# Kernel optimization log

Hardware: AMD Instinct MI355X
Metric: run time of the kernel (lower is better)

## Reference

```python
import jax, jax.numpy as jnp
import numpy as np

N = 65536   # number of input points
M = 4096    # subsample_size (centroids)
K = 64      # group_limit (neighborhood size)
RADIUS = 0.2  # group_radius


def _mlp(x, W1, b1, W2, b2, W3, b3):
    # PyG MLP([6, 64, 64, 128], act='relu'); batch_norm with default running
    # stats (mean 0, var 1) is identity, so: Linear-ReLU-Linear-ReLU-Linear.
    h = jax.nn.relu(x @ W1 + b1)
    h = jax.nn.relu(h @ W2 + b2)
    return h @ W3 + b3


def setup_inputs() -> dict:
    key = jax.random.key(0)
    ks = jax.random.split(key, 8)
    vertices = jax.random.normal(ks[0], (N, 3), dtype=jnp.float32)
    centroid_indices = jax.random.randint(ks[1], (M,), 0, N)

    def lin(k, fi, fo):
        return (jax.random.normal(k, (fi, fo), dtype=jnp.float32) / np.sqrt(fi)).astype(jnp.float32)

    return {
        "vertices": vertices,
        "centroid_indices": centroid_indices,
        "W1": lin(ks[2], 6, 64),  "b1": jnp.zeros((64,), jnp.float32),
        "W2": lin(ks[3], 64, 64), "b2": jnp.zeros((64,), jnp.float32),
        "W3": lin(ks[4], 64, 128), "b3": jnp.zeros((128,), jnp.float32),
    }


def reference(vertices, centroid_indices, W1, b1, W2, b2, W3, b3):
    # --- group_around_centroids ---
    sq_norm = jnp.einsum('ij,ij->i', vertices, vertices)          # [N]
    cpos = vertices[centroid_indices]                              # [M,3]
    # faithful distance formula: sqrt(|sn_c - 2 c.v + sn|)
    d = jnp.sqrt(jnp.abs(sq_norm[centroid_indices][:, None]
                         - 2.0 * (cpos @ vertices.T)
                         + sq_norm[None, :]))                      # [M,N]  (~1 GB)
    # K nearest per centroid (equivalent to masking by k-th sorted distance)
    neg_dk, idx = jax.lax.top_k(-d, K)                             # [M,K]
    d_k = -neg_dk                                                  # ascending distances
    limit = jnp.minimum(d_k[:, K - 1], RADIUS)                     # [M]
    mask = d_k <= limit[:, None]                                   # [M,K]

    # --- PointNetConv: msg = MLP(cat[x_j, pos_j - pos_i]), max-aggregate to centroid ---
    pos_j = vertices[idx]                                          # [M,K,3]
    feat = jnp.concatenate([pos_j, pos_j - cpos[:, None, :]], axis=-1)  # [M,K,6]
    h = _mlp(feat, W1, b1, W2, b2, W3, b3)                         # [M,K,128]
    h = jnp.where(mask[:, :, None], h, -jnp.inf)
    return jnp.max(h, axis=1)                                      # [M,128]
```

## Files before the change

kernel.cpp:

```cpp
#include <hip/hip_runtime.h>
#include <hip/hip_bf16.h>

#define GD     50
#define NC     (GD*GD*GD)
#define CHUNK  250
#define CAPK   256
#define RADIUS_F 0.2f
#define R2SAFE 0.0401f

typedef unsigned long long ull;
typedef __attribute__((ext_vector_type(4))) _Float16 f16x4;
typedef __attribute__((ext_vector_type(8))) _Float16 f16x8;
typedef __attribute__((ext_vector_type(4))) float    f32x4;

__device__ __forceinline__ int cellcoord(float v) {
    int c = (int)floorf((v + 5.0f) * 5.0f);
    return min(max(c, 0), GD - 1);
}


__global__ void sa_zero_kernel(int4* __restrict__ dst, int n4) {
    int i = blockIdx.x * blockDim.x + threadIdx.x;
    int stride = gridDim.x * blockDim.x;
    for (; i < n4; i += stride) dst[i] = make_int4(0, 0, 0, 0);
}

__global__ void sa_count_kernel(const float* __restrict__ vtx,
                                int* __restrict__ cellCnt, int N,
                                const float* __restrict__ W1,
                                const float* __restrict__ W2,
                                const float* __restrict__ W3,
                                _Float16* __restrict__ wf16) {
    int i = blockIdx.x * blockDim.x + threadIdx.x;
    int stride = gridDim.x * blockDim.x;
    for (int p = i; p < N; p += stride) {
        float x = vtx[3 * p], y = vtx[3 * p + 1], z = vtx[3 * p + 2];
        int cc = (cellcoord(z) * GD + cellcoord(y)) * GD + cellcoord(x);
        atomicAdd(&cellCnt[cc], 1);
    }
    for (int e = i; e < 1024; e += stride) {
        int nn = e >> 8, lane = (e >> 2) & 63, j = e & 3;
        int col = nn * 16 + (lane & 15), k = (lane >> 4) * 4 + j;
        wf16[e] = (k < 6) ? (_Float16)W1[k * 64 + col] : (_Float16)0.f;
    }
    for (int e = i; e < 2048; e += stride) {
        int nn = e >> 9, lane = (e >> 3) & 63, j = e & 7;
        int col = nn * 16 + (lane & 15), k = (lane >> 4) * 8 + j;
        wf16[1024 + e] = (_Float16)W2[k * 64 + col];
        wf16[3072 + e] = (_Float16)W2[(k + 32) * 64 + col];
    }
    for (int e = i; e < 4096; e += stride) {
        int nn = e >> 9, lane = (e >> 3) & 63, j = e & 7;
        int col = nn * 16 + (lane & 15), k = (lane >> 4) * 8 + j;
        wf16[5120 + e] = (_Float16)W3[k * 128 + col];
        wf16[9216 + e] = (_Float16)W3[(k + 32) * 128 + col];
    }
}

__global__ __launch_bounds__(256) void sa_offsets_kernel(
    const int* __restrict__ cellCnt, int* __restrict__ cellStart,
    int* __restrict__ cellEnd, int* __restrict__ cellCur,
    int* __restrict__ cursor) {
    __shared__ int sc[256];
    __shared__ int base_s;
    int t = threadIdx.x;
    int i = blockIdx.x * CHUNK + t;
    int c = (t < CHUNK) ? cellCnt[i] : 0;
    sc[t] = c;
    __syncthreads();
    for (int d = 1; d < 256; d <<= 1) {
        int o = (t >= d) ? sc[t - d] : 0;
        __syncthreads();
        sc[t] += o;
        __syncthreads();
    }
    if (t == 255) base_s = atomicAdd(cursor, sc[255]);
    __syncthreads();
    int start = base_s + sc[t] - c;
    if (t < CHUNK) {
        cellStart[i] = start;
        cellEnd[i] = start + c;
        cellCur[i] = start;
    }
}

__global__ void sa_scatter_kernel(const float* __restrict__ vtx,
                                  int* __restrict__ cellCur,
                                  float4* __restrict__ sorted4,
                                  const int* __restrict__ cidx,
                                  float4* __restrict__ cpos4,
                                  int N, int M) {
    int p = blockIdx.x * blockDim.x + threadIdx.x;
    if (p < N) {
        float x = vtx[3 * p], y = vtx[3 * p + 1], z = vtx[3 * p + 2];
        int cc = (cellcoord(z) * GD + cellcoord(y)) * GD + cellcoord(x);
        int pos = atomicAdd(&cellCur[cc], 1);
        sorted4[pos] = make_float4(x, y, z, __int_as_float(p));
    }
    if (p < M) {
        int i = cidx[p];
        float x = vtx[3 * i], y = vtx[3 * i + 1], z = vtx[3 * i + 2];
        float sn = fmaf(z, z, fmaf(y, y, x * x));
        cpos4[p] = make_float4(x, y, z, sn);
    }
}

__global__ __launch_bounds__(64) void sa_collect_kernel(
    const float4* __restrict__ cpos4,
    const float4* __restrict__ sorted4,
    const int* __restrict__ cellStart, const int* __restrict__ cellEnd,
    _Float16* __restrict__ featG, int* __restrict__ nselG) {

    __shared__ __align__(16) ull key[CAPK + 64];
    __shared__ __align__(16) float4 pos_s[CAPK];
    __shared__ int selb[64];
    __shared__ int chdesc[64];
    __shared__ int scnt_s;

    int lane = threadIdx.x;
    int c = blockIdx.x;
    float4 cc = cpos4[c];

    int cx = cellcoord(cc.x), cy = cellcoord(cc.y), cz = cellcoord(cc.z);
    int x0 = max(cx - 1, 0), x1 = min(cx + 1, GD - 1), lx = x1 - x0 + 1;
    int y0 = max(cy - 1, 0), y1 = min(cy + 1, GD - 1), ly = y1 - y0 + 1;
    int z0 = max(cz - 1, 0), z1 = min(cz + 1, GD - 1), lz = z1 - z0 + 1;
    int nrow = ly * lz;

    int rstart = 0, rlen = 0;
    if (lane < nrow) {
        int iy = lane % ly, iz = lane / ly;
        int gy = y0 + iy, gz = z0 + iz;
        float ylo = (gy == 0) ? -1e30f : gy * 0.2f - 5.0f;
        float yhi = (gy == GD - 1) ? 1e30f : (gy + 1) * 0.2f - 5.0f;
        float zlo = (gz == 0) ? -1e30f : gz * 0.2f - 5.0f;
        float zhi = (gz == GD - 1) ? 1e30f : (gz + 1) * 0.2f - 5.0f;
        float dy = fmaxf(0.f, fmaxf(ylo - cc.y, cc.y - yhi));
        float dz = fmaxf(0.f, fmaxf(zlo - cc.z, cc.z - zhi));
        if (fmaf(dz, dz, dy * dy) <= R2SAFE) {
            int cell0 = (gz * GD + gy) * GD + x0;
            int cellL = cell0 + (lx - 1);
            rstart = cellStart[cell0];
            rlen = cellEnd[cellL] - rstart;
        }
    }
    if (lane == 0) scnt_s = 0;

    int nch = (rlen + 63) >> 6;
    int ip = nch;
#pragma unroll
    for (int d = 1; d < 16; d <<= 1) {
        int o = __shfl_up(ip, d);
        if (lane >= d) ip += o;
    }
    int C = __shfl(ip, nrow - 1);
    int ebase = ip - nch;
    if (lane < nrow) {
        for (int k = 0; k < nch; ++k) {
            int st = rstart + (k << 6);
            int ln = min(64, rlen - (k << 6));
            chdesc[ebase + k] = st | (ln << 20);
        }
    }

#pragma unroll 2
    for (int ch = 0; ch < C; ++ch) {
        int d0 = chdesc[ch];
        int st = d0 & 0xFFFFF, ln = d0 >> 20;
        if (lane < ln) {
            int sp = st + lane;
            float4 p = sorted4[sp];
            float psn = fmaf(p.z, p.z, fmaf(p.y, p.y, p.x * p.x));
            float dot = fmaf(p.z, cc.z, fmaf(p.y, cc.y, p.x * cc.x));
            float tt = fmaf(-2.f, dot, cc.w) + psn;
            if (tt <= R2SAFE) {
                float dd = sqrtf(fabsf(tt));
                if (dd <= RADIUS_F) {
                    int pid = __float_as_int(p.w);
                    int slot = atomicAdd(&scnt_s, 1);
                    if (slot < CAPK) {
                        key[slot] = (((ull)__float_as_uint(dd)) << 32) | (unsigned)pid;
                        pos_s[slot] = p;
                    }
                }
            }
        }
    }

    int n = min(scnt_s, CAPK);
    int nsel = min(n, 64);
    int n64 = (n + 63) & ~63;
    if (lane < n64 - n) key[n + lane] = ~0ull;
    if (n > 64) {
        for (int i = lane; i < n; i += 64) {
            ull ki = key[i];
            int r = 0;
            for (int j = 0; j < n64; j += 8) {
#pragma unroll
                for (int jj = 0; jj < 8; ++jj)
                    r += (key[j + jj] < ki) ? 1 : 0;
            }
            if (r < 64) selb[r] = i;
        }
    } else {
        for (int i = lane; i < n; i += 64) selb[i] = i;
    }

    {
        _Float16 z = (_Float16)0.f;
        f16x8 lo8 = {z, z, z, z, z, z, z, z};
        if (lane < nsel) {
            float4 p = pos_s[selb[lane]];
            lo8[0] = (_Float16)p.x; lo8[1] = (_Float16)p.y; lo8[2] = (_Float16)p.z;
            lo8[3] = (_Float16)(p.x - cc.x);
            lo8[4] = (_Float16)(p.y - cc.y);
            lo8[5] = (_Float16)(p.z - cc.z);
        }
        f16x8 hi8 = {z, z, z, z, z, z, z, z};
        _Float16* fr = featG + (size_t)c * 1024 + lane * 16;
        *(f16x8*)(fr + 0) = lo8;
        *(f16x8*)(fr + 8) = hi8;
    }
    if (lane == 0) nselG[c] = nsel;
}

__global__ __launch_bounds__(256) void sa_mlp4_kernel(
    const _Float16* __restrict__ featG, const int* __restrict__ nselG,
    const _Float16* __restrict__ wf16,
    const float* __restrict__ b1, const float* __restrict__ b2,
    const float* __restrict__ b3, float* __restrict__ out) {

    __shared__ __align__(16) _Float16 h1[4096];
    __shared__ __align__(16) _Float16 h2[4096];

    int t = threadIdx.x, w = t >> 6, lane = t & 63;
    int r16 = lane & 15, g = lane >> 4;
    int c = blockIdx.x;
    int nsel = nselG[c];
    const _Float16* fG = featG + (size_t)c * 1024;

    f16x4 F1  = ((const f16x4*)wf16)[w * 64 + lane];
    f16x8 FA2 = ((const f16x8*)(wf16 + 1024))[w * 64 + lane];
    f16x8 FB2 = ((const f16x8*)(wf16 + 3072))[w * 64 + lane];
    f16x8 FA3a = ((const f16x8*)(wf16 + 5120))[(2 * w + 0) * 64 + lane];
    f16x8 FA3b = ((const f16x8*)(wf16 + 5120))[(2 * w + 1) * 64 + lane];
    f16x8 FB3a = ((const f16x8*)(wf16 + 9216))[(2 * w + 0) * 64 + lane];
    f16x8 FB3b = ((const f16x8*)(wf16 + 9216))[(2 * w + 1) * 64 + lane];
    float B1 = b1[w * 16 + r16];
    float B2 = b2[w * 16 + r16];
    float B3a = b3[(2 * w + 0) * 16 + r16];
    float B3b = b3[(2 * w + 1) * 16 + r16];

    {
        f16x4 a1[4];
#pragma unroll
        for (int m = 0; m < 4; ++m)
            a1[m] = *(const f16x4*)&fG[(m * 16 + r16) * 16 + g * 4];
        int col = w * 16 + r16;
#pragma unroll
        for (int m = 0; m < 4; ++m) {
            f32x4 acc = {B1, B1, B1, B1};
            acc = __builtin_amdgcn_mfma_f32_16x16x16f16(a1[m], F1, acc, 0, 0, 0);
#pragma unroll
            for (int reg = 0; reg < 4; ++reg) {
                int row = m * 16 + g * 4 + reg;
                h1[row * 64 + (col ^ ((row & 7) << 3))] =
                    (_Float16)fmaxf(acc[reg], 0.f);
            }
        }
    }
    __syncthreads();

    {
        int col = w * 16 + r16;
#pragma unroll
        for (int m = 0; m < 4; ++m) {
            int row = m * 16 + r16;
            f16x8 aA = *(const f16x8*)&h1[row * 64 + ((g * 8) ^ ((row & 7) << 3))];
            f16x8 aB = *(const f16x8*)&h1[row * 64 + ((32 + g * 8) ^ ((row & 7) << 3))];
            f32x4 acc = {B2, B2, B2, B2};
            acc = __builtin_amdgcn_mfma_f32_16x16x32_f16(aA, FA2, acc, 0, 0, 0);
            acc = __builtin_amdgcn_mfma_f32_16x16x32_f16(aB, FB2, acc, 0, 0, 0);
#pragma unroll
            for (int reg = 0; reg < 4; ++reg) {
                int row2 = m * 16 + g * 4 + reg;
                h2[row2 * 64 + (col ^ ((row2 & 7) << 3))] =
                    (_Float16)fmaxf(acc[reg], 0.f);
            }
        }
    }
    __syncthreads();

    {
        f16x8 a3[4][2];
#pragma unroll
        for (int m = 0; m < 4; ++m)
#pragma unroll
            for (int kt = 0; kt < 2; ++kt) {
                int row = m * 16 + r16;
                int k0 = kt * 32 + g * 8;
                a3[m][kt] = *(const f16x8*)&h2[row * 64 + (k0 ^ ((row & 7) << 3))];
            }
        float ninf = __int_as_float(0xff800000);
#pragma unroll
        for (int q = 0; q < 2; ++q) {
            float bb = q ? B3b : B3a;
            f16x8 fa = q ? FA3b : FA3a;
            f16x8 fb = q ? FB3b : FB3a;
            float vm = ninf;
#pragma unroll
            for (int m = 0; m < 4; ++m) {
                f32x4 acc = {bb, bb, bb, bb};
                acc = __builtin_amdgcn_mfma_f32_16x16x32_f16(a3[m][0], fa, acc, 0, 0, 0);
                acc = __builtin_amdgcn_mfma_f32_16x16x32_f16(a3[m][1], fb, acc, 0, 0, 0);
#pragma unroll
                for (int reg = 0; reg < 4; ++reg) {
                    int row = m * 16 + g * 4 + reg;
                    if (row < nsel) vm = fmaxf(vm, acc[reg]);
                }
            }
            vm = fmaxf(vm, __shfl_xor(vm, 16));
            vm = fmaxf(vm, __shfl_xor(vm, 32));
            if (lane < 16)
                out[(size_t)c * 128 + (2 * w + q) * 16 + lane] = vm;
        }
    }
}

extern "C" void kernel_launch(void* const* d_in, const int* in_sizes, int n_in,
                              void* d_out, int out_size, void* d_ws, size_t ws_size,
                              hipStream_t stream) {
    const float* vtx = (const float*)d_in[0];
    const int* cidx  = (const int*)d_in[1];
    const float* W1  = (const float*)d_in[2];
    const float* b1  = (const float*)d_in[3];
    const float* W2  = (const float*)d_in[4];
    const float* b2  = (const float*)d_in[5];
    const float* W3  = (const float*)d_in[6];
    const float* b3  = (const float*)d_in[7];
    float* out = (float*)d_out;

    int N = in_sizes[0] / 3;
    int M = in_sizes[1];

    char* ws = (char*)d_ws;
    size_t off = 0;
    float4* sorted4 = (float4*)(ws + off); off += (size_t)N * 16;
    float4* cpos4   = (float4*)(ws + off); off += (size_t)M * 16;
    int* cellCnt    = (int*)(ws + off);    off += (size_t)NC * 4;
    int* cursor     = (int*)(ws + off);    off += 16;
    int* cellStart  = (int*)(ws + off);    off += (size_t)NC * 4;
    int* cellEnd    = (int*)(ws + off);    off += (size_t)NC * 4;
    int* cellCur    = (int*)(ws + off);    off += (size_t)NC * 4;
    _Float16* featG = (_Float16*)(ws + off); off += (size_t)M * 1024 * 2;
    int* nselG      = (int*)(ws + off);    off += (size_t)M * 4;
    _Float16* wf16  = (_Float16*)(ws + off);

    sa_zero_kernel<<<256, 256, 0, stream>>>((int4*)cellCnt, (NC * 4 + 16) / 16);
    sa_count_kernel<<<512, 256, 0, stream>>>(vtx, cellCnt, N, W1, W2, W3, wf16);
    sa_offsets_kernel<<<NC / CHUNK, 256, 0, stream>>>(cellCnt, cellStart,
                                                      cellEnd, cellCur, cursor);
    sa_scatter_kernel<<<(N + 255) / 256, 256, 0, stream>>>(vtx, cellCur,
                                                           sorted4, cidx,
                                                           cpos4, N, M);
    sa_collect_kernel<<<M, 64, 0, stream>>>(cpos4, sorted4,
                                            cellStart, cellEnd, featG, nselG);
    sa_mlp4_kernel<<<M, 256, 0, stream>>>(featG, nselG, wf16,
                                          b1, b2, b3, out);
}
```

Baseline: 64.55 us.

## Fuse neighbor collection and MLP into one 256-thread kernel per centroid

Merges the 64-thread collect kernel and the 256-thread MLP kernel into a single kernel per centroid. Features stay in shared memory instead of round-tripping through a global featG buffer, and the neighbor scan and rank selection are spread across four waves instead of one. This removes one launch and the global feature traffic, at the cost of more LDS per block (key, pos_s, featb, h1, h2) and extra block barriers, which may lower occupancy.

```diff
diff --git a/kernel.cpp b/kernel.cpp
--- a/kernel.cpp
+++ b/kernel.cpp
@@ -105,21 +105,29 @@
     }
 }
 
-__global__ __launch_bounds__(64) void sa_collect_kernel(
-    const float4* __restrict__ cpos4,
-    const float4* __restrict__ sorted4,
+__global__ __launch_bounds__(256) void sa_fused4_kernel(
+    const float4* __restrict__ cpos4, const float4* __restrict__ sorted4,
     const int* __restrict__ cellStart, const int* __restrict__ cellEnd,
-    _Float16* __restrict__ featG, int* __restrict__ nselG) {
-
-    __shared__ __align__(16) ull key[CAPK + 64];
+    const _Float16* __restrict__ wf16,
+    const float* __restrict__ b1, const float* __restrict__ b2,
+    const float* __restrict__ b3, float* __restrict__ out) {
+
+    __shared__ __align__(16) ull key[CAPK];
     __shared__ __align__(16) float4 pos_s[CAPK];
+    __shared__ __align__(16) _Float16 featb[1024];
+    __shared__ __align__(16) _Float16 h1[4096];
+    __shared__ __align__(16) _Float16 h2[4096];
     __shared__ int selb[64];
     __shared__ int chdesc[64];
     __shared__ int scnt_s;
 
-    int lane = threadIdx.x;
+    int t = threadIdx.x, w = t >> 6, lane = t & 63;
+    int r16 = lane & 15, g = lane >> 4;
     int c = blockIdx.x;
     float4 cc = cpos4[c];
+
+    key[t] = ~0ull;
+    if (t == 0) scnt_s = 0;
 
     int cx = cellcoord(cc.x), cy = cellcoord(cc.y), cz = cellcoord(cc.z);
     int x0 = max(cx - 1, 0), x1 = min(cx + 1, GD - 1), lx = x1 - x0 + 1;
@@ -144,8 +152,6 @@
             rlen = cellEnd[cellL] - rstart;
         }
     }
-    if (lane == 0) scnt_s = 0;
-
     int nch = (rlen + 63) >> 6;
     int ip = nch;
 #pragma unroll
@@ -155,16 +161,16 @@
     }
     int C = __shfl(ip, nrow - 1);
     int ebase = ip - nch;
-    if (lane < nrow) {
+    if (w == 0 && lane < nrow) {
         for (int k = 0; k < nch; ++k) {
             int st = rstart + (k << 6);
             int ln = min(64, rlen - (k << 6));
             chdesc[ebase + k] = st | (ln << 20);
         }
     }
-
-#pragma unroll 2
-    for (int ch = 0; ch < C; ++ch) {
+    __syncthreads();
+
+    for (int ch = w; ch < C; ch += 4) {
         int d0 = chdesc[ch];
         int st = d0 & 0xFFFFF, ln = d0 >> 20;
         if (lane < ln) {
@@ -186,58 +192,7 @@
             }
         }
     }
-
-    int n = min(scnt_s, CAPK);
-    int nsel = min(n, 64);
-    int n64 = (n + 63) & ~63;
-    if (lane < n64 - n) key[n + lane] = ~0ull;
-    if (n > 64) {
-        for (int i = lane; i < n; i += 64) {
-            ull ki = key[i];
-            int r = 0;
-            for (int j = 0; j < n64; j += 8) {
-#pragma unroll
-                for (int jj = 0; jj < 8; ++jj)
-                    r += (key[j + jj] < ki) ? 1 : 0;
-            }
-            if (r < 64) selb[r] = i;
-        }
-    } else {
-        for (int i = lane; i < n; i += 64) selb[i] = i;
-    }
-
-    {
-        _Float16 z = (_Float16)0.f;
-        f16x8 lo8 = {z, z, z, z, z, z, z, z};
-        if (lane < nsel) {
-            float4 p = pos_s[selb[lane]];
-            lo8[0] = (_Float16)p.x; lo8[1] = (_Float16)p.y; lo8[2] = (_Float16)p.z;
-            lo8[3] = (_Float16)(p.x - cc.x);
-            lo8[4] = (_Float16)(p.y - cc.y);
-            lo8[5] = (_Float16)(p.z - cc.z);
-        }
-        f16x8 hi8 = {z, z, z, z, z, z, z, z};
-        _Float16* fr = featG + (size_t)c * 1024 + lane * 16;
-        *(f16x8*)(fr + 0) = lo8;
-        *(f16x8*)(fr + 8) = hi8;
-    }
-    if (lane == 0) nselG[c] = nsel;
-}
-
-__global__ __launch_bounds__(256) void sa_mlp4_kernel(
-    const _Float16* __restrict__ featG, const int* __restrict__ nselG,
-    const _Float16* __restrict__ wf16,
-    const float* __restrict__ b1, const float* __restrict__ b2,
-    const float* __restrict__ b3, float* __restrict__ out) {
-
-    __shared__ __align__(16) _Float16 h1[4096];
-    __shared__ __align__(16) _Float16 h2[4096];
-
-    int t = threadIdx.x, w = t >> 6, lane = t & 63;
-    int r16 = lane & 15, g = lane >> 4;
-    int c = blockIdx.x;
-    int nsel = nselG[c];
-    const _Float16* fG = featG + (size_t)c * 1024;
+    __syncthreads();
 
     f16x4 F1  = ((const f16x4*)wf16)[w * 64 + lane];
     f16x8 FA2 = ((const f16x8*)(wf16 + 1024))[w * 64 + lane];
@@ -251,11 +206,46 @@
     float B3a = b3[(2 * w + 0) * 16 + r16];
     float B3b = b3[(2 * w + 1) * 16 + r16];
 
+    int n = min(scnt_s, CAPK);
+    int nsel = min(n, 64);
+    int n64 = (n + 63) & ~63;
+    if (n > 64) {
+        for (int i = t; i < n; i += 256) {
+            ull ki = key[i];
+            int r = 0;
+            for (int j = 0; j < n64; j += 8) {
+#pragma unroll
+                for (int jj = 0; jj < 8; ++jj)
+                    r += (key[j + jj] < ki) ? 1 : 0;
+            }
+            if (r < 64) selb[r] = i;
+        }
+    } else {
+        for (int i = t; i < n; i += 256) selb[i] = i;
+    }
+    __syncthreads();
+
+    if (t < 64) {
+        _Float16 z = (_Float16)0.f;
+        f16x8 lo8 = {z, z, z, z, z, z, z, z};
+        if (t < nsel) {
+            float4 p = pos_s[selb[t]];
+            lo8[0] = (_Float16)p.x; lo8[1] = (_Float16)p.y; lo8[2] = (_Float16)p.z;
+            lo8[3] = (_Float16)(p.x - cc.x);
+            lo8[4] = (_Float16)(p.y - cc.y);
+            lo8[5] = (_Float16)(p.z - cc.z);
+        }
+        f16x8 hi8 = {z, z, z, z, z, z, z, z};
+        *(f16x8*)&featb[t * 16 + 0] = lo8;
+        *(f16x8*)&featb[t * 16 + 8] = hi8;
+    }
+    __syncthreads();
+
     {
         f16x4 a1[4];
 #pragma unroll
         for (int m = 0; m < 4; ++m)
-            a1[m] = *(const f16x4*)&fG[(m * 16 + r16) * 16 + g * 4];
+            a1[m] = *(const f16x4*)&featb[(m * 16 + r16) * 16 + g * 4];
         int col = w * 16 + r16;
 #pragma unroll
         for (int m = 0; m < 4; ++m) {
@@ -352,8 +342,6 @@
     int* cellStart  = (int*)(ws + off);    off += (size_t)NC * 4;
     int* cellEnd    = (int*)(ws + off);    off += (size_t)NC * 4;
     int* cellCur    = (int*)(ws + off);    off += (size_t)NC * 4;
-    _Float16* featG = (_Float16*)(ws + off); off += (size_t)M * 1024 * 2;
-    int* nselG      = (int*)(ws + off);    off += (size_t)M * 4;
     _Float16* wf16  = (_Float16*)(ws + off);
 
     sa_zero_kernel<<<256, 256, 0, stream>>>((int4*)cellCnt, (NC * 4 + 16) / 16);
@@ -363,8 +351,7 @@
     sa_scatter_kernel<<<(N + 255) / 256, 256, 0, stream>>>(vtx, cellCur,
                                                            sorted4, cidx,
                                                            cpos4, N, M);
-    sa_collect_kernel<<<M, 64, 0, stream>>>(cpos4, sorted4,
-                                            cellStart, cellEnd, featG, nselG);
-    sa_mlp4_kernel<<<M, 256, 0, stream>>>(featG, nselG, wf16,
-                                          b1, b2, b3, out);
-}
+    sa_fused4_kernel<<<M, 256, 0, stream>>>(cpos4, sorted4,
+                                            cellStart, cellEnd, wf16,
+                                            b1, b2, b3, out);
+}
```

Measured after the change: 61.42 us. -4.9%, faster.
